# Performance work log

Measured on AMD Instinct MI355X. Metric: run time of the kernel, lower is better.

Reference implementation:

```python
import jax, jax.numpy as jnp
import numpy as np
import math

V, L, D, H, S_MAX = 32000, 6, 768, 8, 256
HD = D // H
SCALE_FACTOR = 2  # attn_scale_factor in the original (TUPE-style)
POS_SCALING = float(HD * SCALE_FACTOR) ** (-0.5)
REL_BINS, MAX_DIST = 32, 128


def _rel_pos_bucket_np(rel, num_buckets=REL_BINS, max_distance=MAX_DIST):
    # bidirectional T5-style bucketing (faithful to relative_position_bucket)
    n = -rel
    num_buckets //= 2
    ret = (n < 0).astype(np.int64) * num_buckets
    n = np.abs(n)
    max_exact = num_buckets // 2
    is_small = n < max_exact
    val_if_large = max_exact + (
        np.log(np.maximum(n, 1).astype(np.float32) / max_exact)
        / math.log(max_distance / max_exact) * (num_buckets - max_exact)
    ).astype(np.int64)
    val_if_large = np.minimum(val_if_large, num_buckets - 1)
    ret += np.where(is_small, n, val_if_large)
    return ret


def _layernorm(x, g, b, eps=1e-5):
    mu = jnp.mean(x, axis=-1, keepdims=True)
    var = jnp.var(x, axis=-1, keepdims=True)
    return (x - mu) * jax.lax.rsqrt(var + eps) * g + b


def setup_inputs() -> dict:
    key = jax.random.key(0)
    ks = jax.random.split(key, 16)
    B, S = 32, 256
    init = lambda k, shape: (jax.random.normal(k, shape, jnp.float32) * 0.02)
    pos_idx = np.arange(S)
    rp = _rel_pos_bucket_np(pos_idx[None, :] - pos_idx[:, None])  # [S,S]
    return {
        "tokens": jax.random.randint(ks[0], (B, S), 0, V, dtype=jnp.int32),
        "embed_tokens": init(ks[1], (V, D)),
        "pos_emb": init(ks[2], (S_MAX + 1, D)),
        "pos_q_w": init(ks[3], (D, D)), "pos_q_b": jnp.zeros((D,), jnp.float32),
        "pos_k_w": init(ks[4], (D, D)), "pos_k_b": jnp.zeros((D,), jnp.float32),
        "pos_ln_g": jnp.ones((D,), jnp.float32), "pos_ln_b": jnp.zeros((D,), jnp.float32),
        "rel_bias_table": init(ks[5], (REL_BINS + 1, H)),
        "rp_bucket": jnp.asarray(rp, jnp.int32),
        "Wq": init(ks[6], (L, D, D)), "bq": jnp.zeros((L, D), jnp.float32),
        "Wk": init(ks[7], (L, D, D)), "bk": jnp.zeros((L, D), jnp.float32),
        "Wv": init(ks[8], (L, D, D)), "bv": jnp.zeros((L, D), jnp.float32),
        "Wo": init(ks[9], (L, D, D)), "bo": jnp.zeros((L, D), jnp.float32),
    }


def reference(tokens, embed_tokens, pos_emb, pos_q_w, pos_q_b, pos_k_w, pos_k_b,
              pos_ln_g, pos_ln_b, rel_bias_table, rp_bucket,
              Wq, bq, Wk, bk, Wv, bv, Wo, bo):
    B, S = tokens.shape
    # relative positional bias: bucket lookup -> [H,S,S]
    rel_bias = rel_bias_table[rp_bucket]            # [S,S,H]
    rel_bias = jnp.transpose(rel_bias, (2, 0, 1))   # [H,S,S]
    # absolute positional bias (TUPE): LN(pos) -> per-head q/k -> bmm
    w = _layernorm(pos_emb[:S], pos_ln_g, pos_ln_b)             # [S,D]
    pq = (w @ pos_q_w.T + pos_q_b).reshape(S, H, HD) * POS_SCALING
    pk = (w @ pos_k_w.T + pos_k_b).reshape(S, H, HD)
    abs_bias = jnp.einsum('ihd,jhd->hij', pq, pk)               # [H,S,S]
    bias = (abs_bias + rel_bias)[None]                          # [1,H,S,S]

    x = embed_tokens[tokens]                                    # [B,S,D]
    scale = float(HD * SCALE_FACTOR) ** (-0.5)
    for l in range(L):
        q = (x @ Wq[l].T + bq[l]).reshape(B, S, H, HD) * scale
        k = (x @ Wk[l].T + bk[l]).reshape(B, S, H, HD)
        v = (x @ Wv[l].T + bv[l]).reshape(B, S, H, HD)
        scores = jnp.einsum('bihd,bjhd->bhij', q, k) + bias     # [B,H,S,S]
        attn = jax.nn.softmax(scores, axis=-1)
        o = jnp.einsum('bhij,bjhd->bihd', attn, v).reshape(B, S, D)
        x = o @ Wo[l].T + bo[l]
    return x[:, 0, :]  # sentence rep [B,D]
```

## Files before the change

### kernel.cpp

```cpp
#include <hip/hip_runtime.h>
#include <hip/hip_bf16.h>
#include <math.h>

constexpr int SEQ = 256;
constexpr int DIM = 768;
constexpr int NH  = 8;
constexpr int HD  = 96;

typedef __attribute__((ext_vector_type(8))) short short8;
typedef __attribute__((ext_vector_type(4))) float f32x4;
using bf16 = __hip_bfloat16;

#define ASYNC_COPY16(gptr, lptr) \
  __builtin_amdgcn_global_load_lds((const __attribute__((address_space(1))) void*)(gptr), \
                                   (__attribute__((address_space(3))) void*)(lptr), 16, 0, 0)

__global__ __launch_bounds__(256) void gemm_kernel(
    const float* __restrict__ A, int lda, long aoz,
    const float* __restrict__ W, int ldw, long woz,
    const float* __restrict__ bias, long boz,
    bf16* __restrict__ C, int ldc, long coz,
    int M, int N, int K, float scale,
    const int* __restrict__ rp, const float* __restrict__ rtab)
{
    const int hz = blockIdx.z;
    A += (long)hz * aoz;
    W += (long)hz * woz;
    if (bias) bias += (long)hz * boz;
    C += (long)hz * coz;

    __shared__ float As[16][68];
    __shared__ float Ws[16][68];

    const int bm = blockIdx.y * 64;
    const int bn = blockIdx.x * 64;
    const int tid = threadIdx.x;
    const int tx = tid & 15;
    const int ty = tid >> 4;

    float acc[4][4] = {};

    for (int k0 = 0; k0 < K; k0 += 16) {
#pragma unroll
        for (int i = 0; i < 4; i++) {
            int idx = tid + i * 256;
            int r = idx >> 4, c = idx & 15;
            As[c][r] = A[(long)(bm + r) * lda + (k0 + c)];
            Ws[c][r] = W[(long)(bn + r) * ldw + (k0 + c)];
        }
        __syncthreads();
#pragma unroll
        for (int kk = 0; kk < 16; kk++) {
            const float4 a = *(const float4*)&As[kk][ty * 4];
            const float4 w = *(const float4*)&Ws[kk][tx * 4];
            acc[0][0] += a.x * w.x; acc[0][1] += a.x * w.y; acc[0][2] += a.x * w.z; acc[0][3] += a.x * w.w;
            acc[1][0] += a.y * w.x; acc[1][1] += a.y * w.y; acc[1][2] += a.y * w.z; acc[1][3] += a.y * w.w;
            acc[2][0] += a.z * w.x; acc[2][1] += a.z * w.y; acc[2][2] += a.z * w.z; acc[2][3] += a.z * w.w;
            acc[3][0] += a.w * w.x; acc[3][1] += a.w * w.y; acc[3][2] += a.w * w.z; acc[3][3] += a.w * w.w;
        }
        __syncthreads();
    }

    const int n0 = bn + tx * 4;
    float4 bv = make_float4(0.f, 0.f, 0.f, 0.f);
    if (bias) bv = *(const float4*)&bias[n0];
#pragma unroll
    for (int i = 0; i < 4; i++) {
        const int m = bm + ty * 4 + i;
        float4 r;
        if (rtab) {
            r.x = acc[i][0] * scale + rtab[rp[(n0 + 0) * 256 + m] * 8 + hz];
            r.y = acc[i][1] * scale + rtab[rp[(n0 + 1) * 256 + m] * 8 + hz];
            r.z = acc[i][2] * scale + rtab[rp[(n0 + 2) * 256 + m] * 8 + hz];
            r.w = acc[i][3] * scale + rtab[rp[(n0 + 3) * 256 + m] * 8 + hz];
        } else {
            r.x = (acc[i][0] + bv.x) * scale;
            r.y = (acc[i][1] + bv.y) * scale;
            r.z = (acc[i][2] + bv.z) * scale;
            r.w = (acc[i][3] + bv.w) * scale;
        }
        bf16 t4[4];
        t4[0] = __float2bfloat16(r.x);
        t4[1] = __float2bfloat16(r.y);
        t4[2] = __float2bfloat16(r.z);
        t4[3] = __float2bfloat16(r.w);
        if (rtab) {
            bf16* dst = C + ((long)blockIdx.x * 4 + (tx >> 2)) * 4096
                          + ((long)blockIdx.y * 4 + (ty >> 2)) * 256;
            const int lane2 = (tx & 3) * 16 + ((ty * 4 + i) & 15);
            *(uint2*)&dst[lane2 * 4] = *(uint2*)t4;
        } else {
            *(uint2*)&C[(long)m * ldc + n0] = *(uint2*)t4;
        }
    }
}

constexpr int RB_A = 10368;
constexpr int RB_B = RB_A + 3456;
constexpr int RB_C = RB_B + 54;
constexpr int RB_D = RB_C + 6144;
constexpr int RB_E = RB_D + 256;
constexpr int RB_F = RB_E + 1152;
constexpr int RB_G = RB_F + 2;

__global__ __launch_bounds__(256) void setup_mega_kernel(
    const int* __restrict__ tokens, const float* __restrict__ embed,
    const float* __restrict__ pos_emb,
    const float* __restrict__ pos_q_w, const float* __restrict__ pos_q_b,
    const float* __restrict__ pos_k_w, const float* __restrict__ pos_k_b,
    const float* __restrict__ pos_ln_g, const float* __restrict__ pos_ln_b,
    const float* __restrict__ Wq, const float* __restrict__ Wk,
    const float* __restrict__ Wv, const float* __restrict__ Wo,
    const float* __restrict__ bq, const float* __restrict__ bk,
    const float* __restrict__ bv,
    bf16* __restrict__ wqkv, bf16* __restrict__ woT, float* __restrict__ bqkv,
    bf16* __restrict__ xb, bf16* __restrict__ wln,
    bf16* __restrict__ wsW, float* __restrict__ wsB, float scale)
{
    const int bid = blockIdx.x, tid = threadIdx.x;

    if (bid < RB_A) {
        const long idx = (long)bid * 256 + tid;
        const long e = idx * 4;
        const int k = (int)(e % 768);
        const long nl = e / 768;
        const int n = (int)(nl % 2304);
        const int l = (int)(nl / 2304);
        const float* src;
        float sc = 1.f;
        if (n < 768)       { src = Wq + ((long)l * 768 + n) * 768; sc = scale; }
        else if (n < 1536) { src = Wk + ((long)l * 768 + (n - 768)) * 768; }
        else               { src = Wv + ((long)l * 768 + (n - 1536)) * 768; }
        const float4 v = *(const float4*)&src[k];
        bf16 tmp[4];
        tmp[0] = __float2bfloat16(v.x * sc);
        tmp[1] = __float2bfloat16(v.y * sc);
        tmp[2] = __float2bfloat16(v.z * sc);
        tmp[3] = __float2bfloat16(v.w * sc);
        *(uint2*)&wqkv[((long)l * 2304 + n) * 768 + k] = *(uint2*)tmp;
    } else if (bid < RB_B) {
        __shared__ float t[32][33];
        const int b2 = bid - RB_A;
        const int l = b2 / 576, r2 = b2 % 576;
        const int c0 = (r2 % 24) * 32, j0 = (r2 / 24) * 32;
        const int tx = tid & 31, ty = tid >> 5;
        const float* src = Wo + (long)l * 768 * 768;
#pragma unroll
        for (int rr = 0; rr < 32; rr += 8)
            t[ty + rr][tx] = src[(long)(c0 + ty + rr) * 768 + j0 + tx];
        __syncthreads();
        bf16* dst = woT + (long)l * 768 * 768;
#pragma unroll
        for (int rr = 0; rr < 32; rr += 8)
            dst[(long)(j0 + ty + rr) * 768 + c0 + tx] = __float2bfloat16(t[tx][ty + rr]);
    } else if (bid < RB_C) {
        const int idx = (bid - RB_B) * 256 + tid;
        if (idx < 6 * 2304) {
            const int n = idx % 2304, l = idx / 2304;
            float v;
            if (n < 768)       v = bq[l * 768 + n] * scale;
            else if (n < 1536) v = bk[l * 768 + (n - 768)];
            else               v = bv[l * 768 + (n - 1536)];
            bqkv[idx] = v;
        }
    } else if (bid < RB_D) {
        const int idx = (bid - RB_C) * 256 + tid;
        const int t = idx / 192;
        const int d = idx - t * 192;
        const int tok = tokens[t];
        const float4 v = ((const float4*)(embed + (long)tok * DIM))[d];
        bf16 tmp[4];
        tmp[0] = __float2bfloat16(v.x);
        tmp[1] = __float2bfloat16(v.y);
        tmp[2] = __float2bfloat16(v.z);
        tmp[3] = __float2bfloat16(v.w);
        *(uint2*)&xb[(long)t * DIM + d * 4] = *(uint2*)tmp;
    } else if (bid < RB_E) {
        __shared__ float buf[256];
        const int i = bid - RB_D;
        const float* row = pos_emb + (long)i * DIM;
        float v0 = row[tid], v1 = row[tid + 256], v2 = row[tid + 512];
        buf[tid] = v0 + v1 + v2;
        __syncthreads();
        for (int off = 128; off > 0; off >>= 1) {
            if (tid < off) buf[tid] += buf[tid + off];
            __syncthreads();
        }
        const float mean = buf[0] * (1.f / 768.f);
        __syncthreads();
        const float d0 = v0 - mean, d1 = v1 - mean, d2 = v2 - mean;
        buf[tid] = d0 * d0 + d1 * d1 + d2 * d2;
        __syncthreads();
        for (int off = 128; off > 0; off >>= 1) {
            if (tid < off) buf[tid] += buf[tid + off];
            __syncthreads();
        }
        const float rstd = rsqrtf(buf[0] * (1.f / 768.f) + 1e-5f);
        bf16* wr = wln + (long)i * DIM;
        wr[tid]       = __float2bfloat16(d0 * rstd * pos_ln_g[tid]       + pos_ln_b[tid]);
        wr[tid + 256] = __float2bfloat16(d1 * rstd * pos_ln_g[tid + 256] + pos_ln_b[tid + 256]);
        wr[tid + 512] = __float2bfloat16(d2 * rstd * pos_ln_g[tid + 512] + pos_ln_b[tid + 512]);
    } else if (bid < RB_F) {
        const long idx = (long)(bid - RB_E) * 256 + tid;
        const long e = idx * 4;
        const float4 v = (e < 589824) ? *(const float4*)&pos_q_w[e]
                                      : *(const float4*)&pos_k_w[e - 589824];
        bf16 tmp[4];
        tmp[0] = __float2bfloat16(v.x);
        tmp[1] = __float2bfloat16(v.y);
        tmp[2] = __float2bfloat16(v.z);
        tmp[3] = __float2bfloat16(v.w);
        *(uint2*)&wsW[e] = *(uint2*)tmp;
    } else {
        const int idx = (bid - RB_F) * 256 + tid;
        wsB[idx] = (idx < 768) ? pos_q_b[idx] : pos_k_b[idx - 768];
    }
}

__global__ __launch_bounds__(256) void fused_bias_kernel(
    const bf16* __restrict__ wqkv, const float* __restrict__ bo,
    const float* __restrict__ bqkv, float* __restrict__ bf_)
{
    const int l = blockIdx.y;
    const int lane = threadIdx.x & 63, wave = threadIdx.x >> 6;
    const int nloc = wave * 8 + (lane >> 3);
    const int seg = lane & 7;
    const int n = blockIdx.x * 32 + nloc;
    const bf16* wrow = wqkv + ((long)(l + 1) * 2304 + n) * 768 + seg * 96;
    const float* bsrc = bo + (long)l * 768 + seg * 96;
    float s = 0.f;
#pragma unroll
    for (int c8 = 0; c8 < 12; c8++) {
        const short8 w8 = *(const short8*)&wrow[c8 * 8];
#pragma unroll
        for (int e = 0; e < 8; e++) {
            bf16 b;
            *(short*)&b = w8[e];
            s += __bfloat162float(b) * bsrc[c8 * 8 + e];
        }
    }
    s += __shfl_xor(s, 1);
    s += __shfl_xor(s, 2);
    s += __shfl_xor(s, 4);
    if (seg == 0) bf_[l * 2304 + n] = s + bqkv[(l + 1) * 2304 + n];
}

#define GEMM_PREF(AS, BS, KB)                                                 \
  {                                                                           \
    _Pragma("unroll")                                                         \
    for (int i = 0; i < 2; i++) {                                             \
      const int u = tid + i * 512;                                            \
      const int r = u >> 3, c = u & 7;                                        \
      const int ca = c ^ (r & 7);                                             \
      ASYNC_COPY16(A + (bm + r) * (long)K + (KB) + ca * 8, &AS[u * 8]);       \
      ASYNC_COPY16(B + (bn + r) * (long)K + (KB) + ca * 8, &BS[u * 8]);       \
    }                                                                         \
  }

#define GEMM_COMPUTE(AS, BS)                                                  \
  {                                                                           \
    _Pragma("unroll")                                                         \
    for (int ks = 0; ks < 2; ks++) {                                          \
      const int cc = ks * 4 + quad;                                           \
      short8 af[4], bfr[2];                                                   \
      _Pragma("unroll")                                                       \
      for (int t = 0; t < 4; t++) {                                           \
        const int ra = wm * 64 + t * 16 + col;                                \
        af[t] = *(const short8*)&AS[ra * 64 + ((cc ^ (ra & 7)) * 8)];         \
      }                                                                       \
      _Pragma("unroll")                                                       \
      for (int t = 0; t < 2; t++) {                                           \
        const int rb = wn * 32 + t * 16 + col;                                \
        bfr[t] = *(const short8*)&BS[rb * 64 + ((cc ^ (rb & 7)) * 8)];        \
      }                                                                       \
      _Pragma("unroll")                                                       \
      for (int tm = 0; tm < 4; tm++)                                          \
        _Pragma("unroll")                                                     \
        for (int tn = 0; tn < 2; tn++)                                        \
          acc[tm][tn] = __builtin_amdgcn_mfma_f32_16x16x32_bf16(af[tm], bfr[tn], acc[tm][tn], 0, 0, 0); \
    }                                                                         \
  }

__global__ __launch_bounds__(512, 4) void gemm_bf16_kernel(
    const bf16* __restrict__ A, const bf16* __restrict__ B,
    const float* __restrict__ bias,
    bf16* __restrict__ Cb, bf16* __restrict__ vTout, float* __restrict__ Cf,
    int N, int K, int swz, long az, long bz, long cz, long biasz, int skipQ)
{
    __shared__ bf16 As0[128 * 64];
    __shared__ bf16 Bs0[128 * 64];
    __shared__ bf16 As1[128 * 64];
    __shared__ bf16 Bs1[128 * 64];

    A += (long)blockIdx.z * az;
    B += (long)blockIdx.z * bz;
    if (Cb) Cb += (long)blockIdx.z * cz;
    if (Cf) Cf += (long)blockIdx.z * cz;
    if (bias) bias += (long)blockIdx.z * biasz;

    const int tid = threadIdx.x;
    const int lane = tid & 63, wave = tid >> 6;
    const int wm = wave & 1, wn = wave >> 1;

    int bmt, bnt;
    if (swz) {
        const int id = blockIdx.x + gridDim.x * blockIdx.y;
        const int xcd = id & 7, loc = id >> 3;
        bmt = xcd * 8 + (loc & 7);
        bnt = loc >> 3;
    } else {
        bmt = blockIdx.y;
        bnt = blockIdx.x;
    }
    if (skipQ && bnt < 6 && (bmt & 1)) return;

    const long bm = (long)bmt * 128, bn = (long)bnt * 128;
    const int col = lane & 15, quad = lane >> 4;

    f32x4 acc[4][2] = {};

    GEMM_PREF(As0, Bs0, 0);
    for (int kk = 0; kk < K; kk += 128) {
        __syncthreads();
        GEMM_PREF(As1, Bs1, kk + 64);
        GEMM_COMPUTE(As0, Bs0);
        __syncthreads();
        if (kk + 128 < K) GEMM_PREF(As0, Bs0, kk + 128);
        GEMM_COMPUTE(As1, Bs1);
    }

    const bool toVT = (vTout != nullptr) && (bn >= 1536);

    if (toVT) {
        __syncthreads();
        bf16* tb = (wave < 4 ? As0 : Bs0) + (wave & 3) * 2048;
#pragma unroll
        for (int tn = 0; tn < 2; tn++) {
            const int nl = tn * 16 + col;
            const float bvv = bias[bn + wn * 32 + nl];
#pragma unroll
            for (int tm = 0; tm < 4; tm++) {
                const int mc = tm * 4 + quad;
                bf16 t4[4];
#pragma unroll
                for (int r = 0; r < 4; r++)
                    t4[r] = __float2bfloat16(acc[tm][tn][r] + bvv);
                *(uint2*)&tb[(nl * 16 + (mc ^ (nl & 15))) * 4] = *(uint2*)t4;
            }
        }
        const int b_  = (int)((bm + wm * 64) >> 8);
        const int s0  = (int)((bm + wm * 64) & 255);
        const long nb = bn + wn * 32 - 1536;
#pragma unroll
        for (int it2 = 0; it2 < 8; it2++) {
            const int nl = it2 * 4 + quad;
            const uint2 v = *(const uint2*)&tb[(nl * 16 + (col ^ (nl & 15))) * 4];
            *(uint2*)&vTout[((long)b_ * 768 + nb + nl) * 256 + s0 + col * 4] = v;
        }
    } else if (Cf) {
#pragma unroll
        for (int tn = 0; tn < 2; tn++) {
            const long n = bn + wn * 32 + tn * 16 + col;
            const float bvv = bias ? bias[n] : 0.f;
#pragma unroll
            for (int tm = 0; tm < 4; tm++) {
                const long m0 = bm + wm * 64 + tm * 16 + quad * 4;
#pragma unroll
                for (int r = 0; r < 4; r++)
                    Cf[(m0 + r) * N + n] = acc[tm][tn][r] + bvv;
            }
        }
    } else {
#pragma unroll
        for (int tn = 0; tn < 2; tn++) {
            const long n = bn + wn * 32 + tn * 16 + col;
            const float bvv = bias ? bias[n] : 0.f;
#pragma unroll
            for (int tm = 0; tm < 4; tm++) {
                const long m0 = bm + wm * 64 + tm * 16 + quad * 4;
#pragma unroll
                for (int r = 0; r < 4; r++)
                    Cb[(m0 + r) * N + n] = __float2bfloat16(acc[tm][tn][r] + bvv);
            }
        }
    }
}

#define PREF_K(DST, JC)                                                      \
  { _Pragma("unroll")                                                        \
    for (int i = 0; i < 4; i++) {                                            \
      const int u = tid + i * 256;                                           \
      const int r = u >> 4, pp = u & 15;                                     \
      const int c = pp ^ (r & 15);                                           \
      ASYNC_COPY16(kbase + ((JC) * 64 + r) * 2304 + c * 8, &DST[u * 8]);     \
    } }

#define PREF_V(DST, KC)                                                      \
  { _Pragma("unroll")                                                        \
    for (int i = 0; i < 3; i++) {                                            \
      const int u = tid + i * 256;                                           \
      const int r = u >> 3, pp = u & 7;                                      \
      const int c = pp ^ (r & 7);                                            \
      ASYNC_COPY16(vbase + r * 256 + (KC) * 64 + c * 8, &DST[u * 8]);        \
    } }

#define SCORE(BUF, JC)                                                       \
  { __builtin_amdgcn_s_setprio(1);                                           \
    _Pragma("unroll")                                                        \
    for (int ks = 0; ks < 3; ks++) {                                         \
      _Pragma("unroll")                                                      \
      for (int jt2 = 0; jt2 < 4; jt2++) {                                    \
        const int row = jt2 * 16 + col;                                      \
        const int c = ks * 4 + quad;                                         \
        const short8 bk_ = *(const short8*)&BUF[row * 128 + ((c ^ (row & 15)) * 8)]; \
        accS[(JC) * 4 + jt2] = __builtin_amdgcn_mfma_f32_16x16x32_bf16(aq[ks], bk_, accS[(JC) * 4 + jt2], 0, 0, 0); \
      } }                                                                     \
    __builtin_amdgcn_s_setprio(0); }

#define PV(BUF, PC)                                                          \
  { __builtin_amdgcn_s_setprio(1);                                           \
    _Pragma("unroll")                                                        \
    for (int k2 = 0; k2 < 2; k2++) {                                         \
      const short8 ap = *(const short8*)&Ps[(wave * 16 + col) * PS + (PC) * 64 + k2 * 32 + quad * 8]; \
      _Pragma("unroll")                                                      \
      for (int nt = 0; nt < 6; nt++) {                                       \
        const int row = nt * 16 + col;                                       \
        const int c = k2 * 4 + quad;                                         \
        const short8 bv_ = *(const short8*)&BUF[row * 64 + ((c ^ (row & 7)) * 8)]; \
        accO[nt] = __builtin_amdgcn_mfma_f32_16x16x32_bf16(ap, bv_, accO[nt], 0, 0, 0); \
      } }                                                                     \
    __builtin_amdgcn_s_setprio(0); }

__global__ __launch_bounds__(256, 3) void attn_mfma_kernel(
    const bf16* __restrict__ qkv, const bf16* __restrict__ vT,
    const bf16* __restrict__ biasTp, bf16* __restrict__ o)
{
    constexpr int PS = 136;
    __shared__ bf16 Ps[64 * PS];
    __shared__ bf16 KV0[64 * 128];
    __shared__ bf16 KV1[64 * 128];

    const int blk = blockIdx.x;
    const int h  = blk & 7;
    const int b  = (blk >> 3) & 31;
    const int it = blk >> 8;
    const int i0 = it * 64;
    const int tid = threadIdx.x, lane = tid & 63, wave = tid >> 6;
    const int col = lane & 15, quad = lane >> 4;
    const long rowbase = (long)b * SEQ;

    const bf16* kbase = qkv + rowbase * 2304 + 768 + h * 96;
    const bf16* vbase = vT + ((long)b * 768 + h * 96) * 256;

    PREF_K(KV0, 0);

    short8 aq[3];
    {
        const bf16* qrow = qkv + (rowbase + i0 + wave * 16 + col) * 2304 + h * 96;
#pragma unroll
        for (int ks = 0; ks < 3; ks++)
            aq[ks] = *(const short8*)&qrow[ks * 32 + quad * 8];
    }

    f32x4 accS[16] = {};
    __syncthreads();
    PREF_K(KV1, 1);
    SCORE(KV0, 0);
    __syncthreads();
    PREF_K(KV0, 2);
    SCORE(KV1, 1);
    __syncthreads();
    PREF_K(KV1, 3);
    SCORE(KV0, 2);
    __syncthreads();
    PREF_V(KV0, 0);
    SCORE(KV1, 3);

    {
        const bf16* bbT = biasTp + ((long)(h * 16 + it * 4 + wave) * 4096) + lane * 4;
#pragma unroll
        for (int jt = 0; jt < 16; jt++) {
            bf16 b4[4];
            *(uint2*)b4 = *(const uint2*)&bbT[jt * 256];
            accS[jt][0] += __bfloat162float(b4[0]);
            accS[jt][1] += __bfloat162float(b4[1]);
            accS[jt][2] += __bfloat162float(b4[2]);
            accS[jt][3] += __bfloat162float(b4[3]);
        }
    }

#pragma unroll
    for (int r = 0; r < 4; r++) {
        float t0 = fmaxf(fmaxf(accS[0][r],  accS[1][r]),  accS[2][r]);
        float t1 = fmaxf(fmaxf(accS[3][r],  accS[4][r]),  accS[5][r]);
        float t2 = fmaxf(fmaxf(accS[6][r],  accS[7][r]),  accS[8][r]);
        float t3 = fmaxf(fmaxf(accS[9][r],  accS[10][r]), accS[11][r]);
        float t4 = fmaxf(fmaxf(accS[12][r], accS[13][r]), accS[14][r]);
        float m  = fmaxf(fmaxf(fmaxf(t0, t1), t2), fmaxf(fmaxf(t3, t4), accS[15][r]));
        for (int d = 1; d < 16; d <<= 1) m = fmaxf(m, __shfl_xor(m, d));
        float s = 0.f;
#pragma unroll
        for (int jt = 0; jt < 16; jt++) {
            const float e = __expf(accS[jt][r] - m);
            accS[jt][r] = e;
            s += e;
        }
        for (int d = 1; d < 16; d <<= 1) s += __shfl_xor(s, d);
        const float inv = __builtin_amdgcn_rcpf(s);
#pragma unroll
        for (int jt = 0; jt < 16; jt++) accS[jt][r] *= inv;
        const int prow = wave * 16 + quad * 4 + r;
#pragma unroll
        for (int jt = 0; jt < 8; jt++)
            Ps[prow * PS + jt * 16 + col] = __float2bfloat16(accS[jt][r]);
    }

    f32x4 accO[6] = {};
    __syncthreads();
    PREF_V(KV1, 1);
    PV(KV0, 0);
    __syncthreads();
    PREF_V(KV0, 2);
    PV(KV1, 1);
#pragma unroll
    for (int r = 0; r < 4; r++) {
        const int prow = wave * 16 + quad * 4 + r;
#pragma unroll
        for (int jt = 8; jt < 16; jt++)
            Ps[prow * PS + (jt - 8) * 16 + col] = __float2bfloat16(accS[jt][r]);
    }
    __syncthreads();
    PREF_V(KV1, 3);
    PV(KV0, 0);
    __syncthreads();
    PV(KV1, 1);

#pragma unroll
    for (int nt = 0; nt < 6; nt++)
#pragma unroll
        for (int r = 0; r < 4; r++) {
            const long m = rowbase + i0 + wave * 16 + quad * 4 + r;
            o[m * DIM + h * 96 + nt * 16 + col] = __float2bfloat16(accO[nt][r]);
        }
}

__global__ __launch_bounds__(256) void final_out_kernel(
    const bf16* __restrict__ ob, const float* __restrict__ Wo5,
    const float* __restrict__ bo5, float* __restrict__ out)
{
    __shared__ float os[768];
    const int b = blockIdx.y, ng = blockIdx.x, tid = threadIdx.x;
    const bf16* orow = ob + (long)b * 256 * 768;
    for (int i = tid; i < 768; i += 256) os[i] = __bfloat162float(orow[i]);
    __syncthreads();

    const int n = ng * 32 + (tid >> 3);
    const int seg = tid & 7;
    const float* wrow = Wo5 + (long)n * 768 + seg * 96;
    const float* xs = &os[seg * 96];
    float s = 0.f;
#pragma unroll
    for (int k = 0; k < 96; k += 4) {
        const float4 w = *(const float4*)&wrow[k];
        s += xs[k] * w.x + xs[k + 1] * w.y + xs[k + 2] * w.z + xs[k + 3] * w.w;
    }
    s += __shfl_xor(s, 1);
    s += __shfl_xor(s, 2);
    s += __shfl_xor(s, 4);
    if (seg == 0) out[b * 768 + n] = s + bo5[n];
}

extern "C" void kernel_launch(void* const* d_in, const int* in_sizes, int n_in,
                              void* d_out, int out_size, void* d_ws, size_t ws_size,
                              hipStream_t stream)
{
    const int*   tokens   = (const int*)d_in[0];
    const float* embed    = (const float*)d_in[1];
    const float* pos_emb  = (const float*)d_in[2];
    const float* pos_q_w  = (const float*)d_in[3];
    const float* pos_q_b  = (const float*)d_in[4];
    const float* pos_k_w  = (const float*)d_in[5];
    const float* pos_k_b  = (const float*)d_in[6];
    const float* pos_ln_g = (const float*)d_in[7];
    const float* pos_ln_b = (const float*)d_in[8];
    const float* rel_tab  = (const float*)d_in[9];
    const int*   rp       = (const int*)d_in[10];
    const float* Wq = (const float*)d_in[11];
    const float* bq = (const float*)d_in[12];
    const float* Wk = (const float*)d_in[13];
    const float* bk = (const float*)d_in[14];
    const float* Wv = (const float*)d_in[15];
    const float* bv = (const float*)d_in[16];
    const float* Wo = (const float*)d_in[17];
    const float* bo = (const float*)d_in[18];
    float* out = (float*)d_out;

    char* p = (char*)d_ws;
    auto alloc = [&](size_t bytes) -> char* {
        char* r = p;
        p += (bytes + 255) & ~(size_t)255;
        return r;
    };
    const long NT = 32L * SEQ;

    bf16*  biasT = (bf16*) alloc(8L * SEQ * SEQ * 2);
    bf16*  wlnb  = (bf16*) alloc((long)SEQ * DIM * 2);
    float* pqk   = (float*)alloc(2L * SEQ * DIM * 4);
    bf16*  wsWb  = (bf16*) alloc(2L * 768 * 768 * 2);
    float* wsB   = (float*)alloc(2L * 768 * 4);
    bf16*  xb    = (bf16*) alloc(NT * DIM * 2);
    bf16*  qkv   = (bf16*) alloc(NT * 2304 * 2);
    bf16*  vT    = (bf16*) alloc(NT * DIM * 2);
    bf16*  ob    = (bf16*) alloc(NT * DIM * 2);
    bf16*  wqkv  = (bf16*) alloc(6L * 2304 * 768 * 2);
    bf16*  woT   = (bf16*) alloc(6L * 768 * 768 * 2);
    bf16*  wf    = (bf16*) alloc(5L * 2304 * 768 * 2);
    float* bqkv  = (float*)alloc(6L * 2304 * 4);
    float* bfus  = (float*)alloc(5L * 2304 * 4);

    const float SCALE = 0.07216878364870322f;

    setup_mega_kernel<<<RB_G, 256, 0, stream>>>(
        tokens, embed, pos_emb, pos_q_w, pos_q_b, pos_k_w, pos_k_b,
        pos_ln_g, pos_ln_b, Wq, Wk, Wv, Wo, bq, bk, bv,
        wqkv, woT, bqkv, xb, wlnb, wsWb, wsB, SCALE);

    gemm_bf16_kernel<<<dim3(6, 18, 5), 512, 0, stream>>>(
        wqkv + 2304L * 768, woT, nullptr, wf, nullptr, nullptr, 768, 768, 0,
        2304L * 768, 768L * 768, 2304L * 768, 0, 0);
    fused_bias_kernel<<<dim3(72, 5), 256, 0, stream>>>(wqkv, bo, bqkv, bfus);

    gemm_bf16_kernel<<<dim3(6, 2, 2), 512, 0, stream>>>(
        wlnb, wsWb, wsB, nullptr, nullptr, pqk, 768, 768, 0,
        0, 768L * 768, (long)SEQ * DIM, 768, 0);
    gemm_kernel<<<dim3(4, 4, NH), 256, 0, stream>>>(
        pqk + (long)SEQ * DIM, DIM, HD, pqk, DIM, HD, nullptr, 0,
        biasT, SEQ, (long)SEQ * SEQ, SEQ, SEQ, HD, SCALE, rp, rel_tab);

    gemm_bf16_kernel<<<dim3(18, 64, 1), 512, 0, stream>>>(
        xb, wqkv, bqkv, qkv, vT, nullptr, 2304, 768, 1, 0, 0, 0, 0, 0);
    for (int l = 0; l < 5; l++) {
        attn_mfma_kernel<<<1024, 256, 0, stream>>>(qkv, vT, biasT, ob);
        gemm_bf16_kernel<<<dim3(18, 64, 1), 512, 0, stream>>>(
            ob, wf + (long)l * 2304 * 768, bfus + (long)l * 2304, qkv, vT, nullptr,
            2304, 768, 1, 0, 0, 0, 0, (l == 4) ? 1 : 0);
    }
    attn_mfma_kernel<<<256, 256, 0, stream>>>(qkv, vT, biasT, ob);
    final_out_kernel<<<dim3(24, 32), 256, 0, stream>>>(ob, Wo + 5L * 768 * 768, bo + 5L * 768, out);
}
```

Before: 629.8 us.

## Process a whole (batch, head) per attention block with K/V fully resident in LDS

The attention kernel now launches one 512-thread block per (batch, head) instead of one 256-thread block per 64-row query tile. All of K and V for that head are loaded into shared memory once, and two wave teams each handle two query tiles. This removes the repeated K/V fetches across query-tile blocks and the double-buffered per-chunk syncs. In exchange the block uses roughly 147KB of LDS, which limits each CU to one block, and there is no longer any overlap between the up-front loads and compute. A tile-count argument lets the last layer compute only the first query tile.

Result: faster. 603.5 us (-4.2%).

```diff
diff --git a/kernel.cpp b/kernel.cpp
--- a/kernel.cpp
+++ b/kernel.cpp
@@ -386,38 +386,20 @@
     }
 }
 
-#define PREF_K(DST, JC)                                                      \
-  { _Pragma("unroll")                                                        \
-    for (int i = 0; i < 4; i++) {                                            \
-      const int u = tid + i * 256;                                           \
-      const int r = u >> 4, pp = u & 15;                                     \
-      const int c = pp ^ (r & 15);                                           \
-      ASYNC_COPY16(kbase + ((JC) * 64 + r) * 2304 + c * 8, &DST[u * 8]);     \
-    } }
-
-#define PREF_V(DST, KC)                                                      \
-  { _Pragma("unroll")                                                        \
-    for (int i = 0; i < 3; i++) {                                            \
-      const int u = tid + i * 256;                                           \
-      const int r = u >> 3, pp = u & 7;                                      \
-      const int c = pp ^ (r & 7);                                            \
-      ASYNC_COPY16(vbase + r * 256 + (KC) * 64 + c * 8, &DST[u * 8]);        \
-    } }
-
-#define SCORE(BUF, JC)                                                       \
+#define SCORE_R(JC)                                                          \
   { __builtin_amdgcn_s_setprio(1);                                           \
     _Pragma("unroll")                                                        \
     for (int ks = 0; ks < 3; ks++) {                                         \
       _Pragma("unroll")                                                      \
       for (int jt2 = 0; jt2 < 4; jt2++) {                                    \
-        const int row = jt2 * 16 + col;                                      \
-        const int c = ks * 4 + quad;                                         \
-        const short8 bk_ = *(const short8*)&BUF[row * 128 + ((c ^ (row & 15)) * 8)]; \
-        accS[(JC) * 4 + jt2] = __builtin_amdgcn_mfma_f32_16x16x32_bf16(aq[ks], bk_, accS[(JC) * 4 + jt2], 0, 0, 0); \
+        const int row = (JC) * 64 + jt2 * 16 + col;                          \
+        const int cc = ks * 4 + quad;                                        \
+        const short8 bk_ = *(const short8*)&Ks[row * 128 + ((cc ^ (row & 15)) * 8)]; \
+        accS[(JC) * 4 + jt2] = __builtin_amdgcn_mfma_f32_16x16x32_bf16(aqv[ks], bk_, accS[(JC) * 4 + jt2], 0, 0, 0); \
       } }                                                                     \
     __builtin_amdgcn_s_setprio(0); }
 
-#define PV(BUF, PC)                                                          \
+#define PV_R(KC, PC)                                                         \
   { __builtin_amdgcn_s_setprio(1);                                           \
     _Pragma("unroll")                                                        \
     for (int k2 = 0; k2 < 2; k2++) {                                         \
@@ -426,122 +408,134 @@
       for (int nt = 0; nt < 6; nt++) {                                       \
         const int row = nt * 16 + col;                                       \
         const int c = k2 * 4 + quad;                                         \
-        const short8 bv_ = *(const short8*)&BUF[row * 64 + ((c ^ (row & 7)) * 8)]; \
+        const short8 bv_ = *(const short8*)&Vs[(KC) * 6144 + row * 64 + ((c ^ (row & 7)) * 8)]; \
         accO[nt] = __builtin_amdgcn_mfma_f32_16x16x32_bf16(ap, bv_, accO[nt], 0, 0, 0); \
       } }                                                                     \
     __builtin_amdgcn_s_setprio(0); }
 
-__global__ __launch_bounds__(256, 3) void attn_mfma_kernel(
+__global__ __launch_bounds__(512, 2) void attn_mfma_kernel(
     const bf16* __restrict__ qkv, const bf16* __restrict__ vT,
-    const bf16* __restrict__ biasTp, bf16* __restrict__ o)
+    const bf16* __restrict__ biasTp, bf16* __restrict__ o, int nit)
 {
     constexpr int PS = 136;
-    __shared__ bf16 Ps[64 * PS];
-    __shared__ bf16 KV0[64 * 128];
-    __shared__ bf16 KV1[64 * 128];
+    __shared__ bf16 Ks[256 * 128];
+    __shared__ bf16 Vs[4 * 96 * 64];
+    __shared__ bf16 Ps[128 * PS];
 
     const int blk = blockIdx.x;
     const int h  = blk & 7;
-    const int b  = (blk >> 3) & 31;
-    const int it = blk >> 8;
-    const int i0 = it * 64;
+    const int b  = blk >> 3;
     const int tid = threadIdx.x, lane = tid & 63, wave = tid >> 6;
+    const int team = wave >> 2, wl = wave & 3;
     const int col = lane & 15, quad = lane >> 4;
     const long rowbase = (long)b * SEQ;
 
     const bf16* kbase = qkv + rowbase * 2304 + 768 + h * 96;
     const bf16* vbase = vT + ((long)b * 768 + h * 96) * 256;
 
-    PREF_K(KV0, 0);
-
+    const int it0 = team * 2;
     short8 aq[3];
     {
-        const bf16* qrow = qkv + (rowbase + i0 + wave * 16 + col) * 2304 + h * 96;
+        const bf16* qrow = qkv + (rowbase + it0 * 64 + wl * 16 + col) * 2304 + h * 96;
 #pragma unroll
         for (int ks = 0; ks < 3; ks++)
             aq[ks] = *(const short8*)&qrow[ks * 32 + quad * 8];
     }
 
-    f32x4 accS[16] = {};
+#pragma unroll
+    for (int i = 0; i < 8; i++) {
+        const int u = tid + i * 512;
+        const int r = u >> 4, pp = u & 15;
+        const int c = pp ^ (r & 15);
+        ASYNC_COPY16(kbase + (long)r * 2304 + c * 8, &Ks[u * 8]);
+    }
+#pragma unroll
+    for (int i = 0; i < 6; i++) {
+        const int u = tid + i * 512;
+        const int KC = u / 768;
+        const int w = u - KC * 768;
+        const int r = w >> 3, pp = w & 7;
+        const int c = pp ^ (r & 7);
+        ASYNC_COPY16(vbase + r * 256 + KC * 64 + c * 8, &Vs[u * 8]);
+    }
+
     __syncthreads();
-    PREF_K(KV1, 1);
-    SCORE(KV0, 0);
-    __syncthreads();
-    PREF_K(KV0, 2);
-    SCORE(KV1, 1);
-    __syncthreads();
-    PREF_K(KV1, 3);
-    SCORE(KV0, 2);
-    __syncthreads();
-    PREF_V(KV0, 0);
-    SCORE(KV1, 3);
-
-    {
-        const bf16* bbT = biasTp + ((long)(h * 16 + it * 4 + wave) * 4096) + lane * 4;
-#pragma unroll
-        for (int jt = 0; jt < 16; jt++) {
-            bf16 b4[4];
-            *(uint2*)b4 = *(const uint2*)&bbT[jt * 256];
-            accS[jt][0] += __bfloat162float(b4[0]);
-            accS[jt][1] += __bfloat162float(b4[1]);
-            accS[jt][2] += __bfloat162float(b4[2]);
-            accS[jt][3] += __bfloat162float(b4[3]);
-        }
-    }
-
-#pragma unroll
-    for (int r = 0; r < 4; r++) {
-        float t0 = fmaxf(fmaxf(accS[0][r],  accS[1][r]),  accS[2][r]);
-        float t1 = fmaxf(fmaxf(accS[3][r],  accS[4][r]),  accS[5][r]);
-        float t2 = fmaxf(fmaxf(accS[6][r],  accS[7][r]),  accS[8][r]);
-        float t3 = fmaxf(fmaxf(accS[9][r],  accS[10][r]), accS[11][r]);
-        float t4 = fmaxf(fmaxf(accS[12][r], accS[13][r]), accS[14][r]);
-        float m  = fmaxf(fmaxf(fmaxf(t0, t1), t2), fmaxf(fmaxf(t3, t4), accS[15][r]));
-        for (int d = 1; d < 16; d <<= 1) m = fmaxf(m, __shfl_xor(m, d));
-        float s = 0.f;
-#pragma unroll
-        for (int jt = 0; jt < 16; jt++) {
-            const float e = __expf(accS[jt][r] - m);
-            accS[jt][r] = e;
-            s += e;
-        }
-        for (int d = 1; d < 16; d <<= 1) s += __shfl_xor(s, d);
-        const float inv = __builtin_amdgcn_rcpf(s);
-#pragma unroll
-        for (int jt = 0; jt < 16; jt++) accS[jt][r] *= inv;
-        const int prow = wave * 16 + quad * 4 + r;
-#pragma unroll
-        for (int jt = 0; jt < 8; jt++)
-            Ps[prow * PS + jt * 16 + col] = __float2bfloat16(accS[jt][r]);
-    }
-
-    f32x4 accO[6] = {};
-    __syncthreads();
-    PREF_V(KV1, 1);
-    PV(KV0, 0);
-    __syncthreads();
-    PREF_V(KV0, 2);
-    PV(KV1, 1);
-#pragma unroll
-    for (int r = 0; r < 4; r++) {
-        const int prow = wave * 16 + quad * 4 + r;
-#pragma unroll
-        for (int jt = 8; jt < 16; jt++)
-            Ps[prow * PS + (jt - 8) * 16 + col] = __float2bfloat16(accS[jt][r]);
-    }
-    __syncthreads();
-    PREF_V(KV1, 3);
-    PV(KV0, 0);
-    __syncthreads();
-    PV(KV1, 1);
-
-#pragma unroll
-    for (int nt = 0; nt < 6; nt++)
+
+    auto process = [&](int it, const short8 aqv[3]) {
+        f32x4 accS[16] = {};
+        SCORE_R(0); SCORE_R(1); SCORE_R(2); SCORE_R(3);
+
+        {
+            const bf16* bbT = biasTp + ((long)(h * 16 + it * 4 + wl) * 4096) + lane * 4;
+#pragma unroll
+            for (int jt = 0; jt < 16; jt++) {
+                bf16 b4[4];
+                *(uint2*)b4 = *(const uint2*)&bbT[jt * 256];
+                accS[jt][0] += __bfloat162float(b4[0]);
+                accS[jt][1] += __bfloat162float(b4[1]);
+                accS[jt][2] += __bfloat162float(b4[2]);
+                accS[jt][3] += __bfloat162float(b4[3]);
+            }
+        }
+
 #pragma unroll
         for (int r = 0; r < 4; r++) {
-            const long m = rowbase + i0 + wave * 16 + quad * 4 + r;
-            o[m * DIM + h * 96 + nt * 16 + col] = __float2bfloat16(accO[nt][r]);
-        }
+            float t0 = fmaxf(fmaxf(accS[0][r],  accS[1][r]),  accS[2][r]);
+            float t1 = fmaxf(fmaxf(accS[3][r],  accS[4][r]),  accS[5][r]);
+            float t2 = fmaxf(fmaxf(accS[6][r],  accS[7][r]),  accS[8][r]);
+            float t3 = fmaxf(fmaxf(accS[9][r],  accS[10][r]), accS[11][r]);
+            float t4 = fmaxf(fmaxf(accS[12][r], accS[13][r]), accS[14][r]);
+            float m  = fmaxf(fmaxf(fmaxf(t0, t1), t2), fmaxf(fmaxf(t3, t4), accS[15][r]));
+            for (int d = 1; d < 16; d <<= 1) m = fmaxf(m, __shfl_xor(m, d));
+            float s = 0.f;
+#pragma unroll
+            for (int jt = 0; jt < 16; jt++) {
+                const float e = __expf(accS[jt][r] - m);
+                accS[jt][r] = e;
+                s += e;
+            }
+            for (int d = 1; d < 16; d <<= 1) s += __shfl_xor(s, d);
+            const float inv = __builtin_amdgcn_rcpf(s);
+#pragma unroll
+            for (int jt = 0; jt < 16; jt++) accS[jt][r] *= inv;
+            const int prow = wave * 16 + quad * 4 + r;
+#pragma unroll
+            for (int jt = 0; jt < 8; jt++)
+                Ps[prow * PS + jt * 16 + col] = __float2bfloat16(accS[jt][r]);
+        }
+
+        f32x4 accO[6] = {};
+        PV_R(0, 0);
+        PV_R(1, 1);
+#pragma unroll
+        for (int r = 0; r < 4; r++) {
+            const int prow = wave * 16 + quad * 4 + r;
+#pragma unroll
+            for (int jt = 8; jt < 16; jt++)
+                Ps[prow * PS + (jt - 8) * 16 + col] = __float2bfloat16(accS[jt][r]);
+        }
+        PV_R(2, 0);
+        PV_R(3, 1);
+
+#pragma unroll
+        for (int nt = 0; nt < 6; nt++)
+#pragma unroll
+            for (int r = 0; r < 4; r++) {
+                const long m = rowbase + it * 64 + wl * 16 + quad * 4 + r;
+                o[m * DIM + h * 96 + nt * 16 + col] = __float2bfloat16(accO[nt][r]);
+            }
+    };
+
+    if (it0 < nit) process(it0, aq);
+    const int it1 = it0 + 1;
+    if (it1 < nit) {
+        short8 aq2[3];
+        const bf16* qrow = qkv + (rowbase + it1 * 64 + wl * 16 + col) * 2304 + h * 96;
+#pragma unroll
+        for (int ks = 0; ks < 3; ks++)
+            aq2[ks] = *(const short8*)&qrow[ks * 32 + quad * 8];
+        process(it1, aq2);
+    }
 }
 
 __global__ __launch_bounds__(256) void final_out_kernel(
@@ -640,11 +634,11 @@
     gemm_bf16_kernel<<<dim3(18, 64, 1), 512, 0, stream>>>(
         xb, wqkv, bqkv, qkv, vT, nullptr, 2304, 768, 1, 0, 0, 0, 0, 0);
     for (int l = 0; l < 5; l++) {
-        attn_mfma_kernel<<<1024, 256, 0, stream>>>(qkv, vT, biasT, ob);
+        attn_mfma_kernel<<<256, 512, 0, stream>>>(qkv, vT, biasT, ob, 4);
         gemm_bf16_kernel<<<dim3(18, 64, 1), 512, 0, stream>>>(
             ob, wf + (long)l * 2304 * 768, bfus + (long)l * 2304, qkv, vT, nullptr,
             2304, 768, 1, 0, 0, 0, 0, (l == 4) ? 1 : 0);
     }
-    attn_mfma_kernel<<<256, 256, 0, stream>>>(qkv, vT, biasT, ob);
+    attn_mfma_kernel<<<256, 512, 0, stream>>>(qkv, vT, biasT, ob, 1);
     final_out_kernel<<<dim3(24, 32), 256, 0, stream>>>(ob, Wo + 5L * 768 * 768, bo + 5L * 768, out);
 }
```
